# Performance work log

Measured on AMD Instinct MI355X. Metric: run time of the kernel, lower is better.

Reference implementation:

```python
import jax, jax.numpy as jnp
import numpy as np

B, S, D = 4, 2048, 512
H, DK, DV = 8, 64, 64
DFF = 2048
LN_EPS = 1e-5


def _layernorm(x, g, b):
    mu = jnp.mean(x, axis=-1, keepdims=True)
    var = jnp.mean(jnp.square(x - mu), axis=-1, keepdims=True)
    return (x - mu) * jax.lax.rsqrt(var + LN_EPS) * g + b


def setup_inputs() -> dict:
    key = jax.random.key(0)
    ks = jax.random.split(key, 9)
    def xavier(k, shape):
        fan_out, fan_in = shape
        std = np.sqrt(2.0 / (fan_in + fan_out))
        return jax.random.normal(k, shape, jnp.float32) * std
    GELU_GAIN = 1.85
    return {
        "x": jax.random.normal(ks[0], (B, S, D), jnp.float32),
        "attention_mask": jax.random.randint(ks[1], (B, S), 0, 2).astype(bool),
        "Wq": xavier(ks[2], (H * DK, D)),
        "Wk": xavier(ks[3], (H * DK, D)),
        "Wv": xavier(ks[4], (H * DV, D)),
        "Wp": xavier(ks[5], (D, H * DV)),
        "W1": xavier(ks[6], (DFF, D)) * GELU_GAIN,
        "b1": jnp.zeros((DFF,), jnp.float32),
        "W2": xavier(ks[7], (D, DFF)),
        "b2": jnp.zeros((D,), jnp.float32),
        "ln1_g": jnp.ones((D,), jnp.float32),
        "ln1_b": jnp.zeros((D,), jnp.float32),
        "ln2_g": jnp.ones((D,), jnp.float32),
        "ln2_b": jnp.zeros((D,), jnp.float32),
    }


def reference(x, attention_mask, Wq, Wk, Wv, Wp, W1, b1, W2, b2,
              ln1_g, ln1_b, ln2_g, ln2_b):
    b, s, d = x.shape
    residual = x
    q = (x @ Wq.T).reshape(b, s, H, DK)  # [B,S,H,DK]
    k = (x @ Wk.T).reshape(b, s, H, DK)
    v = (x @ Wv.T).reshape(b, s, H, DV)
    score = jnp.einsum("bshd,bthd->bhst", q, k) * (DK ** -0.5)  # [B,H,S,S]
    # subtractive mask: score -= 100 * not(mask)
    score = score - 100.0 * (~attention_mask)[:, None, None, :].astype(score.dtype)
    p = jax.nn.softmax(score, axis=-1)
    ctx = jnp.einsum("bhst,bthd->bshd", p, v).reshape(b, s, H * DV)
    att = ctx @ Wp.T  # dropout p=0.1 is identity in eval
    h = _layernorm(att + residual, ln1_g, ln1_b)
    ff = jax.nn.gelu(h @ W1.T + b1, approximate=False) @ W2.T + b2
    out = _layernorm(ff + h, ln2_g, ln2_b)
    return out
```

## Files before the change

### kernel.cpp

```cpp
#include <hip/hip_runtime.h>
#include <cstdint>
#include <cstddef>

#define B_ 4
#define S_ 2048
#define D_ 512
#define H_ 8
#define DK_ 64
#define DFF_ 2048

using s16x8  = __attribute__((ext_vector_type(8))) short;
using bf16x8 = __attribute__((ext_vector_type(8))) __bf16;
using f32x4  = __attribute__((ext_vector_type(4))) float;

__device__ __forceinline__ short f2bf(float f) {
  unsigned u = __builtin_bit_cast(unsigned, f);
  u += 0x7FFFu + ((u >> 16) & 1u);
  return (short)(u >> 16);
}
__device__ __forceinline__ float bf2f(short s) {
  unsigned u = ((unsigned)(unsigned short)s) << 16;
  return __builtin_bit_cast(float, u);
}

__device__ __forceinline__ void gl2lds16(const void* g, void* l) {
  __builtin_amdgcn_global_load_lds(
      (const __attribute__((address_space(1))) void*)g,
      (__attribute__((address_space(3))) void*)l, 16, 0, 0);
}

__global__ __launch_bounds__(256)
void cvt_all(const float* __restrict__ x, const float* __restrict__ Wq,
             const float* __restrict__ Wk, const float* __restrict__ Wv,
             const float* __restrict__ Wp, const float* __restrict__ W1,
             const float* __restrict__ W2,
             short* __restrict__ xb, short* __restrict__ wqkv,
             short* __restrict__ wp, short* __restrict__ w1, short* __restrict__ w2) {
  int blk = blockIdx.x;
  const float* src; short* dst; int off;
  if (blk < 4096)      { src = x;  dst = xb;            off = blk; }
  else if (blk < 4352) { src = Wq; dst = wqkv;          off = blk - 4096; }
  else if (blk < 4608) { src = Wk; dst = wqkv + 262144; off = blk - 4352; }
  else if (blk < 4864) { src = Wv; dst = wqkv + 524288; off = blk - 4608; }
  else if (blk < 5120) { src = Wp; dst = wp;            off = blk - 4864; }
  else if (blk < 6144) { src = W1; dst = w1;            off = blk - 5120; }
  else                 { src = W2; dst = w2;            off = blk - 6144; }
  int i = (off * 256 + threadIdx.x) * 4;
  float4 v = *(const float4*)(src + i);
  *(short4*)(dst + i) = make_short4(f2bf(v.x), f2bf(v.y), f2bf(v.z), f2bf(v.w));
}

template <int MODE>
__device__ __forceinline__ void gemm_store(int m0, int n, const f32x4& a,
                                           const float* __restrict__ aux1,
                                           void* out0, void* out1, void* out2,
                                           int M, int N, int bz) {
  if constexpr (MODE == 0) {
    const int bb = m0 >> 11, ss0 = m0 & 2047;
    if (n < 512) {
      short4 pk = make_short4(f2bf(a[0] * 0.18033688f), f2bf(a[1] * 0.18033688f),
                              f2bf(a[2] * 0.18033688f), f2bf(a[3] * 0.18033688f));
      *(short4*)((short*)out0 +
          ((((size_t)bb * H_ + (n >> 6)) * 64 + (n & 63)) * S_ + ss0)) = pk;
    } else if (n >= 1024) {
      const int nn = n - 1024;
      short4 pk = make_short4(f2bf(a[0]), f2bf(a[1]), f2bf(a[2]), f2bf(a[3]));
      *(short4*)((short*)out2 +
          ((((size_t)bb * H_ + (nn >> 6)) * 64 + (nn & 63)) * S_ + ss0)) = pk;
    } else {
      const int nn = n - 512;
      const size_t rowb = ((size_t)bb * H_ + (nn >> 6)) * S_ + ss0;
#pragma unroll
      for (int rr = 0; rr < 4; ++rr)
        ((short*)out1)[(rowb + rr) * 64 + (nn & 63)] = f2bf(a[rr]);
    }
  } else if constexpr (MODE == 1) {
    float* dst = (float*)out0 + (size_t)bz * M * N;
#pragma unroll
    for (int rr = 0; rr < 4; ++rr)
      dst[(size_t)(m0 + rr) * N + n] = a[rr];
  } else {
#pragma unroll
    for (int rr = 0; rr < 4; ++rr) {
      float t = a[rr] + aux1[n];
      float x2 = t * t;
      float t2 = t * (2.3022082f + 0.1029464f * x2);
      float e  = __builtin_amdgcn_exp2f(t2);
      float gl = t - t * __builtin_amdgcn_rcpf(1.0f + e);
      ((short*)out0)[(size_t)(m0 + rr) * N + n] = f2bf(gl);
    }
  }
}

template <int MODE>
__global__ __launch_bounds__(256)
void gemm_bt(const short* __restrict__ A, const short* __restrict__ B,
             int M, int N, int K,
             const float* __restrict__ aux1,
             void* __restrict__ out0, void* __restrict__ out1, void* __restrict__ out2) {
  __shared__ alignas(16) short As[2][128][64];
  __shared__ alignas(16) short Bs[2][128][64];

  const int tid  = threadIdx.x;
  const int lane = tid & 63;
  const int wave = tid >> 6;
  const int quad = lane >> 4;
  const int l16  = lane & 15;
  const int wm   = (wave >> 1) * 64;
  const int wn   = (wave & 1) * 64;
  const int bm   = blockIdx.x * 128;
  const int bn   = blockIdx.y * 128;
  const int Kh   = K / gridDim.z;
  const int koff = blockIdx.z * Kh;

  const int srow8 = lane >> 3;
  const int pb    = lane & 7;

  f32x4 acc[4][4] = {};
  const int nt = Kh >> 6;

#pragma unroll
  for (int i = 0; i < 4; ++i) {
    const int rr = wave * 32 + i * 8 + srow8;
    const int cb = pb ^ (rr & 7);
    gl2lds16(A + (size_t)(bm + rr) * K + koff + cb * 8, &As[0][wave * 32 + i * 8][0]);
    gl2lds16(B + (size_t)(bn + rr) * K + koff + cb * 8, &Bs[0][wave * 32 + i * 8][0]);
  }
  __syncthreads();

  int cur = 0;
  for (int t = 0; t < nt; ++t) {
    if (t + 1 < nt) {
      const int kk = koff + (t + 1) * 64;
#pragma unroll
      for (int i = 0; i < 4; ++i) {
        const int rr = wave * 32 + i * 8 + srow8;
        const int cb = pb ^ (rr & 7);
        gl2lds16(A + (size_t)(bm + rr) * K + kk + cb * 8, &As[cur ^ 1][wave * 32 + i * 8][0]);
        gl2lds16(B + (size_t)(bn + rr) * K + kk + cb * 8, &Bs[cur ^ 1][wave * 32 + i * 8][0]);
      }
    }

#pragma unroll
    for (int c = 0; c < 2; ++c) {
      bf16x8 a[4], b[4];
#pragma unroll
      for (int i = 0; i < 4; ++i) {
        const int row = wm + i * 16 + l16;
        a[i] = __builtin_bit_cast(bf16x8,
            *(const s16x8*)&As[cur][row][(((c * 4 + quad) ^ (row & 7))) * 8]);
      }
#pragma unroll
      for (int j = 0; j < 4; ++j) {
        const int row = wn + j * 16 + l16;
        b[j] = __builtin_bit_cast(bf16x8,
            *(const s16x8*)&Bs[cur][row][(((c * 4 + quad) ^ (row & 7))) * 8]);
      }
#pragma unroll
      for (int i = 0; i < 4; ++i)
#pragma unroll
        for (int j = 0; j < 4; ++j)
          acc[i][j] = __builtin_amdgcn_mfma_f32_16x16x32_bf16(a[i], b[j], acc[i][j], 0, 0, 0);
    }

    __syncthreads();
    cur ^= 1;
  }

#pragma unroll
  for (int i = 0; i < 4; ++i) {
    const int m0 = bm + wm + i * 16 + quad * 4;
#pragma unroll
    for (int j = 0; j < 4; ++j)
      gemm_store<MODE>(m0, bn + wn + j * 16 + l16, acc[i][j], aux1,
                       out0, out1, out2, M, N, blockIdx.z);
  }
}

template <int MODE>
__global__ __launch_bounds__(512)
void gemm256(const short* __restrict__ A, const short* __restrict__ B,
             int M, int N, int K,
             const float* __restrict__ aux1,
             void* __restrict__ out0, void* __restrict__ out1, void* __restrict__ out2) {
  __shared__ alignas(16) short As[2][256][64];
  __shared__ alignas(16) short Bs[2][256][64];

  const int tid  = threadIdx.x;
  const int lane = tid & 63;
  const int wave = tid >> 6;
  const int quad = lane >> 4;
  const int l16  = lane & 15;
  const int wm   = (wave >> 2) * 128;
  const int wn   = (wave & 3) * 64;
  const int bm   = blockIdx.x * 256;
  const int bn   = blockIdx.y * 256;

  const int srow8 = lane >> 3;
  const int pb    = lane & 7;

  f32x4 acc[8][4] = {};
  const int nt = K >> 6;

#pragma unroll
  for (int p = 0; p < 4; ++p) {
    const int rr = p * 64 + wave * 8 + srow8;
    const int cb = pb ^ (rr & 7);
    gl2lds16(A + (size_t)(bm + rr) * K + cb * 8, &As[0][p * 64 + wave * 8][0]);
    gl2lds16(B + (size_t)(bn + rr) * K + cb * 8, &Bs[0][p * 64 + wave * 8][0]);
  }
  __syncthreads();

  int cur = 0;
  for (int t = 0; t < nt; ++t) {
    if (t + 1 < nt) {
      const int kk = (t + 1) * 64;
#pragma unroll
      for (int p = 0; p < 4; ++p) {
        const int rr = p * 64 + wave * 8 + srow8;
        const int cb = pb ^ (rr & 7);
        gl2lds16(A + (size_t)(bm + rr) * K + kk + cb * 8, &As[cur ^ 1][p * 64 + wave * 8][0]);
        gl2lds16(B + (size_t)(bn + rr) * K + kk + cb * 8, &Bs[cur ^ 1][p * 64 + wave * 8][0]);
      }
    }

#pragma unroll
    for (int c = 0; c < 2; ++c) {
      bf16x8 a[8], b[4];
#pragma unroll
      for (int i = 0; i < 8; ++i) {
        const int row = wm + i * 16 + l16;
        a[i] = __builtin_bit_cast(bf16x8,
            *(const s16x8*)&As[cur][row][(((c * 4 + quad) ^ (row & 7))) * 8]);
      }
#pragma unroll
      for (int j = 0; j < 4; ++j) {
        const int row = wn + j * 16 + l16;
        b[j] = __builtin_bit_cast(bf16x8,
            *(const s16x8*)&Bs[cur][row][(((c * 4 + quad) ^ (row & 7))) * 8]);
      }
#pragma unroll
      for (int i = 0; i < 8; ++i)
#pragma unroll
        for (int j = 0; j < 4; ++j)
          acc[i][j] = __builtin_amdgcn_mfma_f32_16x16x32_bf16(a[i], b[j], acc[i][j], 0, 0, 0);
    }

    __syncthreads();
    cur ^= 1;
  }

#pragma unroll
  for (int i = 0; i < 8; ++i) {
    const int m0 = bm + wm + i * 16 + quad * 4;
#pragma unroll
    for (int j = 0; j < 4; ++j)
      gemm_store<MODE>(m0, bn + wn + j * 16 + l16, acc[i][j], aux1,
                       out0, out1, out2, M, N, 0);
  }
}

__global__ __launch_bounds__(512)
void flash_attn_mfma(const short* __restrict__ QTg, const short* __restrict__ Kb,
                     const short* __restrict__ Vtg, const void* __restrict__ mraw,
                     short* __restrict__ ctxb) {
  __shared__ alignas(16) short Ks[64][64];
  __shared__ alignas(16) short Vt[64][64];
  __shared__ alignas(16) short Ps[8][32][64];
  __shared__ alignas(8) unsigned char mbits8[256];
  __shared__ unsigned red[8];

  int flat = (blockIdx.z * 8 + blockIdx.y) * 8 + blockIdx.x;
  flat = (flat & 7) * 32 + (flat >> 3);
  const int b = flat >> 6, h = (flat >> 3) & 7;
  const int q0 = (flat & 7) * 256;

  const int tid = threadIdx.x;
  const int w = tid >> 6, lane = tid & 63;
  const int quad = lane >> 4, l16 = lane & 15;
  const size_t base  = ((size_t)(b * H_ + h)) * S_ * DK_;
  const size_t baseT = ((size_t)(b * H_ + h)) * DK_ * S_;

  {
    const unsigned* mw = (const unsigned*)mraw;
    unsigned v = 0;
#pragma unroll
    for (int i = 0; i < 4; ++i) v |= mw[tid + i * 512];
#pragma unroll
    for (int s = 1; s < 64; s <<= 1) v |= __shfl_xor(v, s);
    if (lane == 0) red[w] = v;
    __syncthreads();
    unsigned f = red[0] | red[1] | red[2] | red[3] |
                 red[4] | red[5] | red[6] | red[7];
    if (tid < 256) {
      unsigned byte = 0;
#pragma unroll
      for (int j = 0; j < 8; ++j) {
        int t = tid * 8 + j;
        int gidx = b * S_ + t;
        int val;
        if ((f & ~1u) == 0u)            val = ((const int*)mraw)[gidx];
        else if (f == 0x3F800000u)      val = (((const float*)mraw)[gidx] != 0.0f);
        else                            val = ((const unsigned char*)mraw)[gidx];
        byte |= (val ? 1u : 0u) << j;
      }
      mbits8[tid] = (unsigned char)byte;
    }
  }

  bf16x8 qa[2][2];
#pragma unroll
  for (int st = 0; st < 2; ++st) {
    const int q = q0 + w * 32 + st * 16 + l16;
#pragma unroll
    for (int c = 0; c < 2; ++c) {
      s16x8 t;
#pragma unroll
      for (int j = 0; j < 8; ++j)
        t[j] = QTg[baseT + (size_t)(c * 32 + quad * 8 + j) * S_ + q];
      qa[st][c] = __builtin_bit_cast(bf16x8, t);
    }
  }

  f32x4 Oc[2][4] = {};
  float li[2] = {};
  const int swz = l16 & 7;

  const int r = tid >> 3, cc = tid & 7;
  const short* kp = Kb  + base  + (size_t)r * 64 + cc * 8;
  const short* vp = Vtg + baseT + (size_t)r * S_ + cc * 8;
  const int ch = ((cc ^ (r & 7)) << 3);

  s16x8 kr = *(const s16x8*)(kp);
  s16x8 vr = *(const s16x8*)(vp);

  for (int t0 = 0; t0 < S_; t0 += 64) {
    __syncthreads();
    *(s16x8*)&Ks[r][ch] = kr;
    *(s16x8*)&Vt[r][ch] = vr;
    __syncthreads();

    if (t0 + 64 < S_) {
      kr = *(const s16x8*)(kp + (size_t)(t0 + 64) * 64);
      vr = *(const s16x8*)(vp + (t0 + 64));
    }

    f32x4 sc[2][4] = {};
    __builtin_amdgcn_s_setprio(1);
#pragma unroll
    for (int c = 0; c < 2; ++c) {
#pragma unroll
      for (int jt = 0; jt < 4; ++jt) {
        bf16x8 kb = __builtin_bit_cast(bf16x8,
            *(const s16x8*)&Ks[jt * 16 + l16][((c * 4 + quad) ^ swz) << 3]);
        sc[0][jt] = __builtin_amdgcn_mfma_f32_16x16x32_bf16(kb, qa[0][c], sc[0][jt], 0, 0, 0);
        sc[1][jt] = __builtin_amdgcn_mfma_f32_16x16x32_bf16(kb, qa[1][c], sc[1][jt], 0, 0, 0);
      }
    }
    __builtin_amdgcn_s_setprio(0);

    const unsigned long long mball =
        *(const unsigned long long*)&mbits8[t0 >> 3];
#pragma unroll
    for (int jt = 0; jt < 4; ++jt) {
      const unsigned m16 = ((unsigned)(mball >> (jt * 16))) >> (quad * 4);
      const int pch = (((jt * 2 + (quad >> 1)) ^ swz) << 3) + (quad & 1) * 4;
#pragma unroll
      for (int st = 0; st < 2; ++st) {
        unsigned uu[4];
#pragma unroll
        for (int rr = 0; rr < 4; ++rr) {
          float pe = __builtin_amdgcn_exp2f(sc[st][jt][rr]);
          unsigned u = __builtin_bit_cast(unsigned, pe) & 0xFFFF0000u;
          u = ((m16 >> rr) & 1u) ? u : 0u;
          li[st] += __builtin_bit_cast(float, u);
          uu[rr] = u;
        }
        *(uint2*)&Ps[w][st * 16 + l16][pch] =
            make_uint2(__builtin_amdgcn_perm(uu[1], uu[0], 0x07060302u),
                       __builtin_amdgcn_perm(uu[3], uu[2], 0x07060302u));
      }
    }

    __builtin_amdgcn_s_setprio(1);
#pragma unroll
    for (int c = 0; c < 2; ++c) {
      bf16x8 pa0 = __builtin_bit_cast(bf16x8,
          *(const s16x8*)&Ps[w][l16][((c * 4 + quad) ^ swz) << 3]);
      bf16x8 pa1 = __builtin_bit_cast(bf16x8,
          *(const s16x8*)&Ps[w][16 + l16][((c * 4 + quad) ^ swz) << 3]);
#pragma unroll
      for (int dt = 0; dt < 4; ++dt) {
        bf16x8 vb = __builtin_bit_cast(bf16x8,
            *(const s16x8*)&Vt[dt * 16 + l16][((c * 4 + quad) ^ swz) << 3]);
        Oc[0][dt] = __builtin_amdgcn_mfma_f32_16x16x32_bf16(pa0, vb, Oc[0][dt], 0, 0, 0);
        Oc[1][dt] = __builtin_amdgcn_mfma_f32_16x16x32_bf16(pa1, vb, Oc[1][dt], 0, 0, 0);
      }
    }
    __builtin_amdgcn_s_setprio(0);
  }

#pragma unroll
  for (int st = 0; st < 2; ++st) {
    float l = li[st];
    l += __shfl_xor(l, 16);
    l += __shfl_xor(l, 32);
#pragma unroll
    for (int rr = 0; rr < 4; ++rr) {
      float lr = __shfl(l, quad * 4 + rr);
      float inv = 1.f / lr;
      const size_t row = (size_t)b * S_ + q0 + w * 32 + st * 16 + quad * 4 + rr;
#pragma unroll
      for (int dt = 0; dt < 4; ++dt)
        ctxb[row * (H_ * DK_) + h * 64 + dt * 16 + l16] = f2bf(Oc[st][dt][rr] * inv);
    }
  }
}

__global__ __launch_bounds__(256)
void ln_fused(const float* __restrict__ p0, const float* __restrict__ p1,
              const float* __restrict__ xres, const short* __restrict__ hres,
              const float* __restrict__ bias,
              const float* __restrict__ g, const float* __restrict__ bb,
              float* __restrict__ out32, short* __restrict__ outb) {
  const int wave = threadIdx.x >> 6, lane = threadIdx.x & 63;
  const int token = blockIdx.x * 4 + wave;
  const size_t off = (size_t)token * D_;
  const int c = lane * 8;

  float v[8];
  {
    float4 a0 = *(const float4*)(p0 + off + c);
    float4 a1 = *(const float4*)(p0 + off + c + 4);
    float4 b0 = *(const float4*)(p1 + off + c);
    float4 b1 = *(const float4*)(p1 + off + c + 4);
    v[0]=a0.x+b0.x; v[1]=a0.y+b0.y; v[2]=a0.z+b0.z; v[3]=a0.w+b0.w;
    v[4]=a1.x+b1.x; v[5]=a1.y+b1.y; v[6]=a1.z+b1.z; v[7]=a1.w+b1.w;
  }
  if (xres) {
    float4 x0 = *(const float4*)(xres + off + c);
    float4 x1 = *(const float4*)(xres + off + c + 4);
    v[0]+=x0.x; v[1]+=x0.y; v[2]+=x0.z; v[3]+=x0.w;
    v[4]+=x1.x; v[5]+=x1.y; v[6]+=x1.z; v[7]+=x1.w;
  }
  if (hres) {
    short4 h0 = *(const short4*)(hres + off + c);
    short4 h1 = *(const short4*)(hres + off + c + 4);
    v[0]+=bf2f(h0.x); v[1]+=bf2f(h0.y); v[2]+=bf2f(h0.z); v[3]+=bf2f(h0.w);
    v[4]+=bf2f(h1.x); v[5]+=bf2f(h1.y); v[6]+=bf2f(h1.z); v[7]+=bf2f(h1.w);
  }
  if (bias) {
    float4 c0 = *(const float4*)(bias + c);
    float4 c1 = *(const float4*)(bias + c + 4);
    v[0]+=c0.x; v[1]+=c0.y; v[2]+=c0.z; v[3]+=c0.w;
    v[4]+=c1.x; v[5]+=c1.y; v[6]+=c1.z; v[7]+=c1.w;
  }

  float sum = 0.f;
#pragma unroll
  for (int i = 0; i < 8; ++i) sum += v[i];
#pragma unroll
  for (int m = 1; m < 64; m <<= 1) sum += __shfl_xor(sum, m);
  float mu = sum * (1.0f / D_);
  float vs = 0.f;
#pragma unroll
  for (int i = 0; i < 8; ++i) { v[i] -= mu; vs += v[i] * v[i]; }
#pragma unroll
  for (int m = 1; m < 64; m <<= 1) vs += __shfl_xor(vs, m);
  float rstd = rsqrtf(vs * (1.0f / D_) + 1e-5f);
#pragma unroll
  for (int i = 0; i < 8; ++i) {
    float val = v[i] * rstd * g[c + i] + bb[c + i];
    if (out32) out32[off + c + i] = val;
    if (outb)  outb[off + c + i] = f2bf(val);
  }
}

constexpr size_t OFF_XB   = 0;
constexpr size_t OFF_WQKV = 8388608;
constexpr size_t OFF_WP   = 9961472;
constexpr size_t OFF_W1   = 10485760;
constexpr size_t OFF_W2   = 12582912;
constexpr size_t OFF_QT   = 14680064;
constexpr size_t OFF_K    = 23068672;
constexpr size_t OFF_VT   = 31457280;
constexpr size_t OFF_CTX  = 39845888;
constexpr size_t OFF_P0   = 48234496;
constexpr size_t OFF_P1   = 65011712;
constexpr size_t OFF_HB   = 81788928;
constexpr size_t OFF_FF1  = 14680064;
constexpr size_t WS_NEED  = 90177536;

extern "C" void kernel_launch(void* const* d_in, const int* in_sizes, int n_in,
                              void* d_out, int out_size, void* d_ws, size_t ws_size,
                              hipStream_t stream) {
  if (ws_size < WS_NEED) return;

  const float* x    = (const float*)d_in[0];
  const void*  msk  = d_in[1];
  const float* Wq   = (const float*)d_in[2];
  const float* Wk   = (const float*)d_in[3];
  const float* Wv   = (const float*)d_in[4];
  const float* Wp   = (const float*)d_in[5];
  const float* W1   = (const float*)d_in[6];
  const float* b1   = (const float*)d_in[7];
  const float* W2   = (const float*)d_in[8];
  const float* b2   = (const float*)d_in[9];
  const float* ln1g = (const float*)d_in[10];
  const float* ln1b = (const float*)d_in[11];
  const float* ln2g = (const float*)d_in[12];
  const float* ln2b = (const float*)d_in[13];

  char* ws = (char*)d_ws;
  short* xb    = (short*)(ws + OFF_XB);
  short* wqkv  = (short*)(ws + OFF_WQKV);
  short* Wpb   = (short*)(ws + OFF_WP);
  short* W1b   = (short*)(ws + OFF_W1);
  short* W2b   = (short*)(ws + OFF_W2);
  short* QTb   = (short*)(ws + OFF_QT);
  short* Kbh   = (short*)(ws + OFF_K);
  short* VTb   = (short*)(ws + OFF_VT);
  short* ctxb  = (short*)(ws + OFF_CTX);
  float* p0    = (float*)(ws + OFF_P0);
  short* hb    = (short*)(ws + OFF_HB);
  short* ff1b  = (short*)(ws + OFF_FF1);

  cvt_all<<<7168, 256, 0, stream>>>(x, Wq, Wk, Wv, Wp, W1, W2,
                                    xb, wqkv, Wpb, W1b, W2b);

  gemm256<0><<<dim3(32, 6, 1), 512, 0, stream>>>(xb, wqkv, 8192, 1536, 512,
                                                 nullptr, QTb, Kbh, VTb);

  flash_attn_mfma<<<dim3(S_ / 256, H_, B_), 512, 0, stream>>>(QTb, Kbh, VTb, msk, ctxb);

  gemm_bt<1><<<dim3(64, 4, 2), 256, 0, stream>>>(ctxb, Wpb, 8192, 512, 512,
                                                 nullptr, p0, nullptr, nullptr);

  ln_fused<<<2048, 256, 0, stream>>>(p0, p0 + (size_t)8192 * 512, x, nullptr, nullptr,
                                     ln1g, ln1b, nullptr, hb);

  gemm256<2><<<dim3(32, 8, 1), 512, 0, stream>>>(hb, W1b, 8192, 2048, 512,
                                                 b1, ff1b, nullptr, nullptr);

  gemm_bt<1><<<dim3(64, 4, 2), 256, 0, stream>>>(ff1b, W2b, 8192, 512, 2048,
                                                 nullptr, p0, nullptr, nullptr);

  ln_fused<<<2048, 256, 0, stream>>>(p0, p0 + (size_t)8192 * 512, nullptr, hb, b2,
                                     ln2g, ln2b, (float*)d_out, nullptr);
}
```

Measured before the change: 280.3 us.

## Deepen gemm256 pipeline to four-stage K=32 ring with async waits

```diff
diff --git a/kernel.cpp b/kernel.cpp
--- a/kernel.cpp
+++ b/kernel.cpp
@@ -183,8 +183,8 @@
              int M, int N, int K,
              const float* __restrict__ aux1,
              void* __restrict__ out0, void* __restrict__ out1, void* __restrict__ out2) {
-  __shared__ alignas(16) short As[2][256][64];
-  __shared__ alignas(16) short Bs[2][256][64];
+  __shared__ alignas(16) short As[4][256][32];
+  __shared__ alignas(16) short Bs[4][256][32];
 
   const int tid  = threadIdx.x;
   const int lane = tid & 63;
@@ -196,59 +196,65 @@
   const int bm   = blockIdx.x * 256;
   const int bn   = blockIdx.y * 256;
 
-  const int srow8 = lane >> 3;
-  const int pb    = lane & 7;
+  const int r16 = lane >> 2;
+  const int pc  = lane & 3;
 
   f32x4 acc[8][4] = {};
-  const int nt = K >> 6;
-
-#pragma unroll
-  for (int p = 0; p < 4; ++p) {
-    const int rr = p * 64 + wave * 8 + srow8;
-    const int cb = pb ^ (rr & 7);
-    gl2lds16(A + (size_t)(bm + rr) * K + cb * 8, &As[0][p * 64 + wave * 8][0]);
-    gl2lds16(B + (size_t)(bn + rr) * K + cb * 8, &Bs[0][p * 64 + wave * 8][0]);
-  }
-  __syncthreads();
-
-  int cur = 0;
+  const int nt = K >> 5;
+
+#define STAGE256(t)                                                          \
+  {                                                                          \
+    const int s_ = (t) & 3;                                                  \
+    const int k0_ = (t) * 32;                                                \
+    _Pragma("unroll")                                                        \
+    for (int i_ = 0; i_ < 2; ++i_) {                                         \
+      const int row_ = wave * 32 + i_ * 16 + r16;                            \
+      const int ca_ = pc ^ ((row_ >> 1) & 3);                                \
+      gl2lds16(A + (size_t)(bm + row_) * K + k0_ + ca_ * 8,                  \
+               &As[s_][wave * 32 + i_ * 16][0]);                             \
+      gl2lds16(B + (size_t)(bn + row_) * K + k0_ + ca_ * 8,                  \
+               &Bs[s_][wave * 32 + i_ * 16][0]);                             \
+    }                                                                        \
+  }
+
+  STAGE256(0);
+  STAGE256(1);
+  asm volatile("s_waitcnt vmcnt(4)" ::: "memory");
+  __builtin_amdgcn_s_barrier();
+  __builtin_amdgcn_sched_barrier(0);
+
   for (int t = 0; t < nt; ++t) {
-    if (t + 1 < nt) {
-      const int kk = (t + 1) * 64;
-#pragma unroll
-      for (int p = 0; p < 4; ++p) {
-        const int rr = p * 64 + wave * 8 + srow8;
-        const int cb = pb ^ (rr & 7);
-        gl2lds16(A + (size_t)(bm + rr) * K + kk + cb * 8, &As[cur ^ 1][p * 64 + wave * 8][0]);
-        gl2lds16(B + (size_t)(bn + rr) * K + kk + cb * 8, &Bs[cur ^ 1][p * 64 + wave * 8][0]);
-      }
-    }
-
-#pragma unroll
-    for (int c = 0; c < 2; ++c) {
-      bf16x8 a[8], b[4];
-#pragma unroll
-      for (int i = 0; i < 8; ++i) {
-        const int row = wm + i * 16 + l16;
-        a[i] = __builtin_bit_cast(bf16x8,
-            *(const s16x8*)&As[cur][row][(((c * 4 + quad) ^ (row & 7))) * 8]);
-      }
-#pragma unroll
-      for (int j = 0; j < 4; ++j) {
-        const int row = wn + j * 16 + l16;
-        b[j] = __builtin_bit_cast(bf16x8,
-            *(const s16x8*)&Bs[cur][row][(((c * 4 + quad) ^ (row & 7))) * 8]);
-      }
-#pragma unroll
-      for (int i = 0; i < 8; ++i)
-#pragma unroll
-        for (int j = 0; j < 4; ++j)
-          acc[i][j] = __builtin_amdgcn_mfma_f32_16x16x32_bf16(a[i], b[j], acc[i][j], 0, 0, 0);
-    }
-
-    __syncthreads();
-    cur ^= 1;
-  }
+    if (t + 2 < nt) STAGE256(t + 2);
+    const int s = t & 3;
+
+    bf16x8 a[8], b[4];
+#pragma unroll
+    for (int i = 0; i < 8; ++i) {
+      const int row = wm + i * 16 + l16;
+      a[i] = __builtin_bit_cast(bf16x8,
+          *(const s16x8*)&As[s][row][(quad ^ ((row >> 1) & 3)) * 8]);
+    }
+#pragma unroll
+    for (int j = 0; j < 4; ++j) {
+      const int row = wn + j * 16 + l16;
+      b[j] = __builtin_bit_cast(bf16x8,
+          *(const s16x8*)&Bs[s][row][(quad ^ ((row >> 1) & 3)) * 8]);
+    }
+
+    __builtin_amdgcn_s_setprio(1);
+#pragma unroll
+    for (int i = 0; i < 8; ++i)
+#pragma unroll
+      for (int j = 0; j < 4; ++j)
+        acc[i][j] = __builtin_amdgcn_mfma_f32_16x16x32_bf16(a[i], b[j], acc[i][j], 0, 0, 0);
+    __builtin_amdgcn_s_setprio(0);
+
+    if (t + 2 < nt) asm volatile("s_waitcnt vmcnt(4)" ::: "memory");
+    else            asm volatile("s_waitcnt vmcnt(0)" ::: "memory");
+    __builtin_amdgcn_s_barrier();
+    __builtin_amdgcn_sched_barrier(0);
+  }
+#undef STAGE256
 
 #pragma unroll
   for (int i = 0; i < 8; ++i) {
```

New measurement: 287.9 us. 2.7% more time.

## Drop split-K fp32 partials; write bf16 GEMM outputs with 8-wave blocks

Applied to the files above, without the earlier changes.

```diff
diff --git a/kernel.cpp b/kernel.cpp
--- a/kernel.cpp
+++ b/kernel.cpp
@@ -54,7 +54,7 @@
 __device__ __forceinline__ void gemm_store(int m0, int n, const f32x4& a,
                                            const float* __restrict__ aux1,
                                            void* out0, void* out1, void* out2,
-                                           int M, int N, int bz) {
+                                           int M, int N) {
   if constexpr (MODE == 0) {
     const int bb = m0 >> 11, ss0 = m0 & 2047;
     if (n < 512) {
@@ -74,11 +74,6 @@
       for (int rr = 0; rr < 4; ++rr)
         ((short*)out1)[(rowb + rr) * 64 + (nn & 63)] = f2bf(a[rr]);
     }
-  } else if constexpr (MODE == 1) {
-    float* dst = (float*)out0 + (size_t)bz * M * N;
-#pragma unroll
-    for (int rr = 0; rr < 4; ++rr)
-      dst[(size_t)(m0 + rr) * N + n] = a[rr];
   } else {
 #pragma unroll
     for (int rr = 0; rr < 4; ++rr) {
@@ -92,12 +87,9 @@
   }
 }
 
-template <int MODE>
-__global__ __launch_bounds__(256)
-void gemm_bt(const short* __restrict__ A, const short* __restrict__ B,
-             int M, int N, int K,
-             const float* __restrict__ aux1,
-             void* __restrict__ out0, void* __restrict__ out1, void* __restrict__ out2) {
+__global__ __launch_bounds__(512)
+void gemm_out_bf16(const short* __restrict__ A, const short* __restrict__ B,
+                   int M, int N, int K, short* __restrict__ out) {
   __shared__ alignas(16) short As[2][128][64];
   __shared__ alignas(16) short Bs[2][128][64];
 
@@ -106,46 +98,44 @@
   const int wave = tid >> 6;
   const int quad = lane >> 4;
   const int l16  = lane & 15;
-  const int wm   = (wave >> 1) * 64;
+  const int wm   = (wave >> 1) * 32;
   const int wn   = (wave & 1) * 64;
   const int bm   = blockIdx.x * 128;
   const int bn   = blockIdx.y * 128;
-  const int Kh   = K / gridDim.z;
-  const int koff = blockIdx.z * Kh;
 
   const int srow8 = lane >> 3;
   const int pb    = lane & 7;
 
-  f32x4 acc[4][4] = {};
-  const int nt = Kh >> 6;
-
-#pragma unroll
-  for (int i = 0; i < 4; ++i) {
-    const int rr = wave * 32 + i * 8 + srow8;
+  f32x4 acc[2][4] = {};
+  const int nt = K >> 6;
+
+#pragma unroll
+  for (int i = 0; i < 2; ++i) {
+    const int rr = wave * 16 + i * 8 + srow8;
     const int cb = pb ^ (rr & 7);
-    gl2lds16(A + (size_t)(bm + rr) * K + koff + cb * 8, &As[0][wave * 32 + i * 8][0]);
-    gl2lds16(B + (size_t)(bn + rr) * K + koff + cb * 8, &Bs[0][wave * 32 + i * 8][0]);
+    gl2lds16(A + (size_t)(bm + rr) * K + cb * 8, &As[0][wave * 16 + i * 8][0]);
+    gl2lds16(B + (size_t)(bn + rr) * K + cb * 8, &Bs[0][wave * 16 + i * 8][0]);
   }
   __syncthreads();
 
   int cur = 0;
   for (int t = 0; t < nt; ++t) {
     if (t + 1 < nt) {
-      const int kk = koff + (t + 1) * 64;
-#pragma unroll
-      for (int i = 0; i < 4; ++i) {
-        const int rr = wave * 32 + i * 8 + srow8;
+      const int kk = (t + 1) * 64;
+#pragma unroll
+      for (int i = 0; i < 2; ++i) {
+        const int rr = wave * 16 + i * 8 + srow8;
         const int cb = pb ^ (rr & 7);
-        gl2lds16(A + (size_t)(bm + rr) * K + kk + cb * 8, &As[cur ^ 1][wave * 32 + i * 8][0]);
-        gl2lds16(B + (size_t)(bn + rr) * K + kk + cb * 8, &Bs[cur ^ 1][wave * 32 + i * 8][0]);
+        gl2lds16(A + (size_t)(bm + rr) * K + kk + cb * 8, &As[cur ^ 1][wave * 16 + i * 8][0]);
+        gl2lds16(B + (size_t)(bn + rr) * K + kk + cb * 8, &Bs[cur ^ 1][wave * 16 + i * 8][0]);
       }
     }
 
 #pragma unroll
     for (int c = 0; c < 2; ++c) {
-      bf16x8 a[4], b[4];
-#pragma unroll
-      for (int i = 0; i < 4; ++i) {
+      bf16x8 a[2], b[4];
+#pragma unroll
+      for (int i = 0; i < 2; ++i) {
         const int row = wm + i * 16 + l16;
         a[i] = __builtin_bit_cast(bf16x8,
             *(const s16x8*)&As[cur][row][(((c * 4 + quad) ^ (row & 7))) * 8]);
@@ -157,7 +147,7 @@
             *(const s16x8*)&Bs[cur][row][(((c * 4 + quad) ^ (row & 7))) * 8]);
       }
 #pragma unroll
-      for (int i = 0; i < 4; ++i)
+      for (int i = 0; i < 2; ++i)
 #pragma unroll
         for (int j = 0; j < 4; ++j)
           acc[i][j] = __builtin_amdgcn_mfma_f32_16x16x32_bf16(a[i], b[j], acc[i][j], 0, 0, 0);
@@ -168,12 +158,15 @@
   }
 
 #pragma unroll
-  for (int i = 0; i < 4; ++i) {
+  for (int i = 0; i < 2; ++i) {
     const int m0 = bm + wm + i * 16 + quad * 4;
 #pragma unroll
-    for (int j = 0; j < 4; ++j)
-      gemm_store<MODE>(m0, bn + wn + j * 16 + l16, acc[i][j], aux1,
-                       out0, out1, out2, M, N, blockIdx.z);
+    for (int j = 0; j < 4; ++j) {
+      const int n = bn + wn + j * 16 + l16;
+#pragma unroll
+      for (int rr = 0; rr < 4; ++rr)
+        out[(size_t)(m0 + rr) * N + n] = f2bf(acc[i][j][rr]);
+    }
   }
 }
 
@@ -256,7 +249,7 @@
 #pragma unroll
     for (int j = 0; j < 4; ++j)
       gemm_store<MODE>(m0, bn + wn + j * 16 + l16, acc[i][j], aux1,
-                       out0, out1, out2, M, N, 0);
+                       out0, out1, out2, M, N);
   }
 }
 
@@ -420,6 +413,7 @@
 __global__ __launch_bounds__(256)
 void ln_fused(const float* __restrict__ p0, const float* __restrict__ p1,
               const float* __restrict__ xres, const short* __restrict__ hres,
+              const short* __restrict__ hres2,
               const float* __restrict__ bias,
               const float* __restrict__ g, const float* __restrict__ bb,
               float* __restrict__ out32, short* __restrict__ outb) {
@@ -428,14 +422,14 @@
   const size_t off = (size_t)token * D_;
   const int c = lane * 8;
 
-  float v[8];
-  {
+  float v[8] = {0.f, 0.f, 0.f, 0.f, 0.f, 0.f, 0.f, 0.f};
+  if (p0) {
     float4 a0 = *(const float4*)(p0 + off + c);
     float4 a1 = *(const float4*)(p0 + off + c + 4);
     float4 b0 = *(const float4*)(p1 + off + c);
     float4 b1 = *(const float4*)(p1 + off + c + 4);
-    v[0]=a0.x+b0.x; v[1]=a0.y+b0.y; v[2]=a0.z+b0.z; v[3]=a0.w+b0.w;
-    v[4]=a1.x+b1.x; v[5]=a1.y+b1.y; v[6]=a1.z+b1.z; v[7]=a1.w+b1.w;
+    v[0]+=a0.x+b0.x; v[1]+=a0.y+b0.y; v[2]+=a0.z+b0.z; v[3]+=a0.w+b0.w;
+    v[4]+=a1.x+b1.x; v[5]+=a1.y+b1.y; v[6]+=a1.z+b1.z; v[7]+=a1.w+b1.w;
   }
   if (xres) {
     float4 x0 = *(const float4*)(xres + off + c);
@@ -446,6 +440,12 @@
   if (hres) {
     short4 h0 = *(const short4*)(hres + off + c);
     short4 h1 = *(const short4*)(hres + off + c + 4);
+    v[0]+=bf2f(h0.x); v[1]+=bf2f(h0.y); v[2]+=bf2f(h0.z); v[3]+=bf2f(h0.w);
+    v[4]+=bf2f(h1.x); v[5]+=bf2f(h1.y); v[6]+=bf2f(h1.z); v[7]+=bf2f(h1.w);
+  }
+  if (hres2) {
+    short4 h0 = *(const short4*)(hres2 + off + c);
+    short4 h1 = *(const short4*)(hres2 + off + c + 4);
     v[0]+=bf2f(h0.x); v[1]+=bf2f(h0.y); v[2]+=bf2f(h0.z); v[3]+=bf2f(h0.w);
     v[4]+=bf2f(h1.x); v[5]+=bf2f(h1.y); v[6]+=bf2f(h1.z); v[7]+=bf2f(h1.w);
   }
@@ -485,8 +485,8 @@
 constexpr size_t OFF_K    = 23068672;
 constexpr size_t OFF_VT   = 31457280;
 constexpr size_t OFF_CTX  = 39845888;
-constexpr size_t OFF_P0   = 48234496;
-constexpr size_t OFF_P1   = 65011712;
+constexpr size_t OFF_ATT  = 48234496;
+constexpr size_t OFF_FF2  = 65011712;
 constexpr size_t OFF_HB   = 81788928;
 constexpr size_t OFF_FF1  = 14680064;
 constexpr size_t WS_NEED  = 90177536;
@@ -521,7 +521,8 @@
   short* Kbh   = (short*)(ws + OFF_K);
   short* VTb   = (short*)(ws + OFF_VT);
   short* ctxb  = (short*)(ws + OFF_CTX);
-  float* p0    = (float*)(ws + OFF_P0);
+  short* attb  = (short*)(ws + OFF_ATT);
+  short* ff2b  = (short*)(ws + OFF_FF2);
   short* hb    = (short*)(ws + OFF_HB);
   short* ff1b  = (short*)(ws + OFF_FF1);
 
@@ -533,18 +534,16 @@
 
   flash_attn_mfma<<<dim3(S_ / 256, H_, B_), 512, 0, stream>>>(QTb, Kbh, VTb, msk, ctxb);
 
-  gemm_bt<1><<<dim3(64, 4, 2), 256, 0, stream>>>(ctxb, Wpb, 8192, 512, 512,
-                                                 nullptr, p0, nullptr, nullptr);
-
-  ln_fused<<<2048, 256, 0, stream>>>(p0, p0 + (size_t)8192 * 512, x, nullptr, nullptr,
+  gemm_out_bf16<<<dim3(64, 4, 1), 512, 0, stream>>>(ctxb, Wpb, 8192, 512, 512, attb);
+
+  ln_fused<<<2048, 256, 0, stream>>>(nullptr, nullptr, x, attb, nullptr, nullptr,
                                      ln1g, ln1b, nullptr, hb);
 
   gemm256<2><<<dim3(32, 8, 1), 512, 0, stream>>>(hb, W1b, 8192, 2048, 512,
                                                  b1, ff1b, nullptr, nullptr);
 
-  gemm_bt<1><<<dim3(64, 4, 2), 256, 0, stream>>>(ff1b, W2b, 8192, 512, 2048,
-                                                 nullptr, p0, nullptr, nullptr);
-
-  ln_fused<<<2048, 256, 0, stream>>>(p0, p0 + (size_t)8192 * 512, nullptr, hb, b2,
+  gemm_out_bf16<<<dim3(64, 4, 1), 512, 0, stream>>>(ff1b, W2b, 8192, 512, 2048, ff2b);
+
+  ln_fused<<<2048, 256, 0, stream>>>(nullptr, nullptr, nullptr, hb, ff2b, b2,
                                      ln2g, ln2b, (float*)d_out, nullptr);
 }
```

After: 283.1 us. About the same (+1.0%).

## Use triple-buffered direct global-to-LDS K/V staging in flash attention

Applied to the files above, without the earlier changes.

```diff
diff --git a/kernel.cpp b/kernel.cpp
--- a/kernel.cpp
+++ b/kernel.cpp
@@ -264,8 +264,8 @@
 void flash_attn_mfma(const short* __restrict__ QTg, const short* __restrict__ Kb,
                      const short* __restrict__ Vtg, const void* __restrict__ mraw,
                      short* __restrict__ ctxb) {
-  __shared__ alignas(16) short Ks[64][64];
-  __shared__ alignas(16) short Vt[64][64];
+  __shared__ alignas(16) short Kring[3][64][64];
+  __shared__ alignas(16) short Vring[3][64][64];
   __shared__ alignas(16) short Ps[8][32][64];
   __shared__ alignas(8) unsigned char mbits8[256];
   __shared__ unsigned red[8];
@@ -327,23 +327,24 @@
   const int swz = l16 & 7;
 
   const int r = tid >> 3, cc = tid & 7;
-  const short* kp = Kb  + base  + (size_t)r * 64 + cc * 8;
-  const short* vp = Vtg + baseT + (size_t)r * S_ + cc * 8;
-  const int ch = ((cc ^ (r & 7)) << 3);
-
-  s16x8 kr = *(const s16x8*)(kp);
-  s16x8 vr = *(const s16x8*)(vp);
-
-  for (int t0 = 0; t0 < S_; t0 += 64) {
-    __syncthreads();
-    *(s16x8*)&Ks[r][ch] = kr;
-    *(s16x8*)&Vt[r][ch] = vr;
-    __syncthreads();
-
-    if (t0 + 64 < S_) {
-      kr = *(const s16x8*)(kp + (size_t)(t0 + 64) * 64);
-      vr = *(const s16x8*)(vp + (t0 + 64));
-    }
+  const int scc = cc ^ (r & 7);
+  const short* kpg = Kb  + base  + (size_t)r * 64 + scc * 8;
+  const short* vpg = Vtg + baseT + (size_t)r * S_ + scc * 8;
+
+#define STAGEKV(TT, SL)                                              \
+  gl2lds16(kpg + (size_t)(TT) * 4096, &Kring[SL][w * 8][0]);         \
+  gl2lds16(vpg + (TT) * 64,           &Vring[SL][w * 8][0]);
+
+  STAGEKV(0, 0)
+  STAGEKV(1, 1)
+  asm volatile("s_waitcnt lgkmcnt(0)" ::: "memory");
+  asm volatile("s_waitcnt vmcnt(2)" ::: "memory");
+  __builtin_amdgcn_s_barrier();
+  __builtin_amdgcn_sched_barrier(0);
+
+  int sl0 = 0, sl1 = 1, sl2 = 2;
+  for (int t = 0; t < S_ / 64; ++t) {
+    if (t + 2 < S_ / 64) { STAGEKV(t + 2, sl2) }
 
     f32x4 sc[2][4] = {};
     __builtin_amdgcn_s_setprio(1);
@@ -352,7 +353,7 @@
 #pragma unroll
       for (int jt = 0; jt < 4; ++jt) {
         bf16x8 kb = __builtin_bit_cast(bf16x8,
-            *(const s16x8*)&Ks[jt * 16 + l16][((c * 4 + quad) ^ swz) << 3]);
+            *(const s16x8*)&Kring[sl0][jt * 16 + l16][((c * 4 + quad) ^ swz) << 3]);
         sc[0][jt] = __builtin_amdgcn_mfma_f32_16x16x32_bf16(kb, qa[0][c], sc[0][jt], 0, 0, 0);
         sc[1][jt] = __builtin_amdgcn_mfma_f32_16x16x32_bf16(kb, qa[1][c], sc[1][jt], 0, 0, 0);
       }
@@ -360,7 +361,7 @@
     __builtin_amdgcn_s_setprio(0);
 
     const unsigned long long mball =
-        *(const unsigned long long*)&mbits8[t0 >> 3];
+        *(const unsigned long long*)&mbits8[t * 8];
 #pragma unroll
     for (int jt = 0; jt < 4; ++jt) {
       const unsigned m16 = ((unsigned)(mball >> (jt * 16))) >> (quad * 4);
@@ -392,13 +393,20 @@
 #pragma unroll
       for (int dt = 0; dt < 4; ++dt) {
         bf16x8 vb = __builtin_bit_cast(bf16x8,
-            *(const s16x8*)&Vt[dt * 16 + l16][((c * 4 + quad) ^ swz) << 3]);
+            *(const s16x8*)&Vring[sl0][dt * 16 + l16][((c * 4 + quad) ^ swz) << 3]);
         Oc[0][dt] = __builtin_amdgcn_mfma_f32_16x16x32_bf16(pa0, vb, Oc[0][dt], 0, 0, 0);
         Oc[1][dt] = __builtin_amdgcn_mfma_f32_16x16x32_bf16(pa1, vb, Oc[1][dt], 0, 0, 0);
       }
     }
     __builtin_amdgcn_s_setprio(0);
-  }
+
+    if (t + 2 < S_ / 64) asm volatile("s_waitcnt vmcnt(2)" ::: "memory");
+    else                 asm volatile("s_waitcnt vmcnt(0)" ::: "memory");
+    __builtin_amdgcn_s_barrier();
+    __builtin_amdgcn_sched_barrier(0);
+    int tmp = sl0; sl0 = sl1; sl1 = sl2; sl2 = tmp;
+  }
+#undef STAGEKV
 
 #pragma unroll
   for (int st = 0; st < 2; ++st) {
```

Result: slower. 288.5 us (+2.9%).
